# Optimization experiments

Measured on AMD Instinct MI355X. Metric: run time of the kernel, lower is better.

The kernel has to match this reference:

```python
import jax, jax.numpy as jnp
import numpy as np

N = 50000        # nodes
E = 800000       # edges
MUL = 32         # multiplicity per irrep (32x0e + 32x1o)
NSPEC = 4        # atom species (node_attrs one-hot width)
NBESSEL = 8      # edge_embedding basis size
HID = 8          # invariant_neurons
WNUM = 4 * MUL   # tp.weight_numel (4 'uvu' paths x 32)


def setup_inputs() -> dict:
    key = jax.random.key(0)
    ks = jax.random.split(key, 13)
    return {
        "edge_embedding": jax.random.normal(ks[0], (E, NBESSEL), jnp.float32),
        "node_attrs": jax.random.uniform(ks[1], (N, NSPEC), jnp.float32),
        "node_features": jax.random.normal(ks[2], (N, MUL * 4), jnp.float32),
        "edge_index": jax.random.randint(ks[3], (2, E), 0, N, jnp.int64),
        "edge_attrs": jax.random.normal(ks[4], (E, 4), jnp.float32),
        # linear_1 (per-irrep channel mixing)
        "W1_s": jax.random.normal(ks[5], (MUL, MUL), jnp.float32),
        "W1_v": jax.random.normal(ks[6], (MUL, MUL), jnp.float32),
        # fc: [8] -> [8] -> [128]
        "Wfc1": jax.random.normal(ks[7], (NBESSEL, HID), jnp.float32),
        "Wfc2": jax.random.normal(ks[8], (HID, WNUM), jnp.float32),
        # linear_2: 64x0e+64x1o -> 32x0e+32x1o
        "W2_s": jax.random.normal(ks[9], (2 * MUL, MUL), jnp.float32),
        "W2_v": jax.random.normal(ks[10], (2 * MUL, MUL), jnp.float32),
        # sc: FullyConnectedTensorProduct(32x0e+32x1o, 4x0e -> 32x0e+32x1o)
        "Wsc_s": jax.random.normal(ks[11], (MUL, NSPEC, MUL), jnp.float32),
        "Wsc_v": jax.random.normal(ks[12], (MUL, NSPEC, MUL), jnp.float32),
    }


def reference(edge_embedding, node_attrs, node_features, edge_index, edge_attrs,
              W1_s, W1_v, Wfc1, Wfc2, W2_s, W2_v, Wsc_s, Wsc_v):
    s = node_features[:, :MUL]                       # [N,32] 0e
    v = node_features[:, MUL:].reshape(N, MUL, 3)    # [N,32,3] 1o

    # self-connection: FullyConnectedTensorProduct(features, node_attrs)
    inv = 1.0 / np.sqrt(MUL * NSPEC).astype(np.float32)
    sc_s = jnp.einsum('nu,nz,uzv->nv', s, node_attrs, Wsc_s) * inv
    sc_v = jnp.einsum('nui,nz,uzv->nvi', v, node_attrs, Wsc_v) * inv

    # linear_1 (equivariant: mixes channels within each irrep)
    lin = np.float32(1.0 / np.sqrt(MUL))
    s1 = (s @ W1_s) * lin
    v1 = jnp.einsum('nui,uv->nvi', v, W1_v) * lin

    # fc MLP on edge_embedding -> per-edge TP weights [E,128]
    h = jax.nn.silu((edge_embedding @ Wfc1) * np.float32(1.0 / np.sqrt(NBESSEL)))
    w = (h @ Wfc2) * np.float32(1.0 / np.sqrt(HID))
    w0, w1, w2, w3 = w[:, :MUL], w[:, MUL:2*MUL], w[:, 2*MUL:3*MUL], w[:, 3*MUL:]

    ctr, nbr = edge_index[0], edge_index[1]
    xs = s1[nbr]            # [E,32] gathered scalars
    xv = v1[nbr]            # [E,32,3] gathered vectors
    es = edge_attrs[:, :1]  # [E,1]  edge 0e
    ev = edge_attrs[:, 1:4] # [E,3]  edge 1o

    # weighted CG tensor product ('uvu', per-edge weights)
    out_s0 = w0 * xs * es                                              # 0e x 0e -> 0e
    out_s3 = w3 * jnp.einsum('eui,ei->eu', xv, ev) * np.float32(1/np.sqrt(3))  # 1o x 1o -> 0e
    out_v1 = (w1 * xs)[:, :, None] * ev[:, None, :]                    # 0e x 1o -> 1o
    out_v2 = (w2 * es)[:, :, None] * xv                                # 1o x 0e -> 1o

    e_s = jnp.concatenate([out_s0, out_s3], axis=1)    # [E,64]
    e_v = jnp.concatenate([out_v1, out_v2], axis=1)    # [E,64,3]

    # scatter-sum back to center nodes
    n_s = jax.ops.segment_sum(e_s, ctr, num_segments=N)
    n_v = jax.ops.segment_sum(e_v.reshape(E, -1), ctr, num_segments=N).reshape(N, 2*MUL, 3)

    # linear_2 + residual self-connection
    lin2 = np.float32(1.0 / np.sqrt(2 * MUL))
    out_s = (n_s @ W2_s) * lin2 + sc_s
    out_v = jnp.einsum('nui,uv->nvi', n_v, W2_v) * lin2 + sc_v

    return jnp.concatenate([out_s, out_v.reshape(N, MUL * 3)], axis=1)
```

## Files before the change

### kernel.cpp

```cpp
#include <hip/hip_runtime.h>

#define N_NODES 50000
#define E_EDGES 800000
#define MUL 32
#define CAP 48

__device__ __forceinline__ unsigned bfpack2(float a, float b) {
    unsigned ua = __float_as_uint(a), ub = __float_as_uint(b);
    ua = (ua + 0x7FFFu + ((ua >> 16) & 1u)) >> 16;
    ub = (ub + 0x7FFFu + ((ub >> 16) & 1u)) >> 16;
    return ua | (ub << 16);
}
__device__ __forceinline__ float bflo(unsigned p) { return __uint_as_float(p << 16); }
__device__ __forceinline__ float bfhi(unsigned p) { return __uint_as_float(p & 0xFFFF0000u); }

__global__ __launch_bounds__(256) void edge_prep(
    const float* __restrict__ ee, const float* __restrict__ Wfc1,
    const int* __restrict__ ei, const float* __restrict__ ea,
    int* __restrict__ cnt, uint4* __restrict__ rec)
{
    __shared__ float sW[64];
    if (threadIdx.x < 64) sW[threadIdx.x] = Wfc1[threadIdx.x];
    __syncthreads();
    long long e = (long long)blockIdx.x * 256 + threadIdx.x;
    if (e >= E_EDGES) return;

    int c = ei[e];
    int nbr = ei[E_EDGES + e];
    int slot = atomicAdd(&cnt[c], 1);

    const float4* p = (const float4*)(ee + e * 8);
    float4 a = p[0], b = p[1];
    float emb[8] = {a.x, a.y, a.z, a.w, b.x, b.y, b.z, b.w};
    const float sfc = 0.35355339059327373f;
    float h[8];
#pragma unroll
    for (int k = 0; k < 8; ++k) {
        float acc = 0.f;
#pragma unroll
        for (int t = 0; t < 8; ++t) acc += emb[t] * sW[t * 8 + k];
        acc *= sfc;
        h[k] = acc / (1.f + __expf(-acc));
    }
    float4 av = ((const float4*)ea)[e];

    if (slot < CAP) {
        long long idx = (long long)(c * CAP + slot) * 2;
        uint4 A, B;
        A.x = (unsigned)nbr;
        A.y = bfpack2(h[0], h[1]); A.z = bfpack2(h[2], h[3]); A.w = bfpack2(h[4], h[5]);
        B.x = bfpack2(h[6], h[7]);
        B.y = bfpack2(av.x, av.y); B.z = bfpack2(av.z, av.w);
        B.w = 0u;
        rec[idx] = A;
        rec[idx + 1] = B;
    }
}

__global__ __launch_bounds__(512) void node_pre_sc(
    const float* __restrict__ nf, const float* __restrict__ attrs,
    const float* __restrict__ W1s, const float* __restrict__ W1v,
    const float* __restrict__ Wscs, const float* __restrict__ Wscv,
    uint2* __restrict__ xq, float* __restrict__ out)
{
    __shared__ float sW1s[1024];
    __shared__ float sW1v[1024];
    __shared__ float sWscs[4096];
    __shared__ float sWscv[4096];
    __shared__ float snf[16][128];
    __shared__ float sat[16][4];
    for (int i = threadIdx.x; i < 1024; i += 512) { sW1s[i] = W1s[i]; sW1v[i] = W1v[i]; }
    for (int i = threadIdx.x; i < 4096; i += 512) { sWscs[i] = Wscs[i]; sWscv[i] = Wscv[i]; }
    int g = threadIdx.x >> 5, v = threadIdx.x & 31;
    const float lin = 0.17677669529663687f;
    const float inv = 0.08838834764831845f;
    for (int node0 = blockIdx.x * 16; node0 < N_NODES; node0 += gridDim.x * 16) {
        __syncthreads();
        for (int i = threadIdx.x; i < 16 * 128; i += 512) {
            int nn = node0 + (i >> 7);
            snf[i >> 7][i & 127] = (nn < N_NODES) ? nf[(long long)nn * 128 + (i & 127)] : 0.f;
        }
        if (threadIdx.x < 64) {
            int nn = node0 + (threadIdx.x >> 2);
            sat[threadIdx.x >> 2][threadIdx.x & 3] = (nn < N_NODES) ? attrs[nn * 4 + (threadIdx.x & 3)] : 0.f;
        }
        __syncthreads();
        int n = node0 + g;
        if (n >= N_NODES) continue;
        float az0 = sat[g][0], az1 = sat[g][1], az2 = sat[g][2], az3 = sat[g][3];
        float acc_s = 0.f, a0 = 0.f, a1 = 0.f, a2 = 0.f;
        float scs = 0.f, scv0 = 0.f, scv1 = 0.f, scv2 = 0.f;
#pragma unroll
        for (int u = 0; u < 32; ++u) {
            float su = snf[g][u];
            float x0 = snf[g][32 + u * 3 + 0];
            float x1 = snf[g][32 + u * 3 + 1];
            float x2 = snf[g][32 + u * 3 + 2];
            acc_s += su * sW1s[u * 32 + v];
            float wv = sW1v[u * 32 + v];
            a0 += x0 * wv; a1 += x1 * wv; a2 += x2 * wv;
            int base = u * 128 + v;
            float cs = az0 * sWscs[base] + az1 * sWscs[base + 32] + az2 * sWscs[base + 64] + az3 * sWscs[base + 96];
            scs += su * cs;
            float cv = az0 * sWscv[base] + az1 * sWscv[base + 32] + az2 * sWscv[base + 64] + az3 * sWscv[base + 96];
            scv0 += x0 * cv; scv1 += x1 * cv; scv2 += x2 * cv;
        }
        uint2 q;
        q.x = bfpack2(acc_s * lin, a0 * lin);
        q.y = bfpack2(a1 * lin, a2 * lin);
        xq[n * 32 + v] = q;
        long long ob = (long long)n * 128;
        out[ob + v] = scs * inv;
        out[ob + 32 + v * 3 + 0] = scv0 * inv;
        out[ob + 32 + v * 3 + 1] = scv1 * inv;
        out[ob + 32 + v * 3 + 2] = scv2 * inv;
    }
}

__global__ __launch_bounds__(256, 6) void gather(
    const int* __restrict__ cnt, const uint4* __restrict__ rec,
    const uint2* __restrict__ xq, const float* __restrict__ Wfc2,
    float4* __restrict__ m4)
{
    int wid = threadIdx.x >> 6;
    int lane = threadIdx.x & 63;
    int u = lane & 31;
    int half = lane >> 5;
    const float sfc = 0.35355339059327373f;
    const float is3 = 0.5773502691896258f;
    float wf0[8], wf1[8], wf2[8], wf3[8];
#pragma unroll
    for (int t = 0; t < 8; ++t) {
        wf0[t] = Wfc2[t * 128 + u] * sfc;
        wf1[t] = Wfc2[t * 128 + 32 + u] * sfc;
        wf2[t] = Wfc2[t * 128 + 64 + u] * sfc;
        wf3[t] = Wfc2[t * 128 + 96 + u] * sfc;
    }
    for (int n = blockIdx.x * 4 + wid; n < N_NODES; n += gridDim.x * 4) {
        int deg = cnt[n];
        if (deg > CAP) deg = CAP;
        int T = (deg + 1) >> 1;
        long long base = (long long)n * CAP;
        int nbr_all = (lane < deg) ? (int)rec[(base + lane) * 2].x : 0;
        float as0 = 0.f, as3 = 0.f;
        float av10 = 0.f, av11 = 0.f, av12 = 0.f;
        float av20 = 0.f, av21 = 0.f, av22 = 0.f;
        uint4 A_c = {0, 0, 0, 0}, B_c = {0, 0, 0, 0};
        uint2 q_c = {0, 0};
        float m_c = 0.f;
        if (T > 0) {
            int j = half;
            m_c = (j < deg) ? 1.f : 0.f;
            int js = (j < deg) ? j : 0;
            int nbr = __shfl(nbr_all, js);
            A_c = rec[(base + js) * 2];
            B_c = rec[(base + js) * 2 + 1];
            q_c = xq[nbr * 32 + u];
        }
        for (int t = 0; t < T; ++t) {
            uint4 A_n = {0, 0, 0, 0}, B_n = {0, 0, 0, 0};
            uint2 q_n = {0, 0};
            float m_n = 0.f;
            if (t + 1 < T) {
                int j = 2 * (t + 1) + half;
                m_n = (j < deg) ? 1.f : 0.f;
                int js = (j < deg) ? j : 0;
                int nbr = __shfl(nbr_all, js);
                A_n = rec[(base + js) * 2];
                B_n = rec[(base + js) * 2 + 1];
                q_n = xq[nbr * 32 + u];
            }
            float hh[8] = {bflo(A_c.y), bfhi(A_c.y), bflo(A_c.z), bfhi(A_c.z),
                           bflo(A_c.w), bfhi(A_c.w), bflo(B_c.x), bfhi(B_c.x)};
            float w0 = 0.f, w1 = 0.f, w2 = 0.f, w3 = 0.f;
#pragma unroll
            for (int t8 = 0; t8 < 8; ++t8) {
                float ht = hh[t8];
                w0 += ht * wf0[t8];
                w1 += ht * wf1[t8];
                w2 += ht * wf2[t8];
                w3 += ht * wf3[t8];
            }
            w0 *= m_c; w1 *= m_c; w2 *= m_c; w3 *= m_c;
            float es  = bflo(B_c.y), ev0 = bfhi(B_c.y);
            float ev1 = bflo(B_c.z), ev2 = bfhi(B_c.z);
            float xs  = bflo(q_c.x), xv0 = bfhi(q_c.x);
            float xv1 = bflo(q_c.y), xv2 = bfhi(q_c.y);
            as0 += w0 * xs * es;
            as3 += w3 * (xv0 * ev0 + xv1 * ev1 + xv2 * ev2);
            float t1 = w1 * xs;
            float t2 = w2 * es;
            av10 += t1 * ev0; av11 += t1 * ev1; av12 += t1 * ev2;
            av20 += t2 * xv0; av21 += t2 * xv1; av22 += t2 * xv2;
            A_c = A_n; B_c = B_n; q_c = q_n; m_c = m_n;
        }
        as0  += __shfl_xor(as0, 32);
        as3  += __shfl_xor(as3, 32);
        av10 += __shfl_xor(av10, 32);
        av11 += __shfl_xor(av11, 32);
        av12 += __shfl_xor(av12, 32);
        av20 += __shfl_xor(av20, 32);
        av21 += __shfl_xor(av21, 32);
        av22 += __shfl_xor(av22, 32);
        if (half == 0) m4[(long long)n * 64 + u]      = make_float4(av10, av11, av12, as0);
        else           m4[(long long)n * 64 + 32 + u] = make_float4(av20, av21, av22, as3 * is3);
    }
}

__global__ __launch_bounds__(512) void node_post(
    const float4* __restrict__ m4,
    const float* __restrict__ W2s, const float* __restrict__ W2v,
    float* __restrict__ out)
{
    __shared__ float sW2s[2048];
    __shared__ float sW2v[2048];
    __shared__ float4 sm[16][64];
    for (int i = threadIdx.x; i < 2048; i += 512) { sW2s[i] = W2s[i]; sW2v[i] = W2v[i]; }
    int g = threadIdx.x >> 5, v = threadIdx.x & 31;
    const float lin2 = 0.125f;
    for (int node0 = blockIdx.x * 16; node0 < N_NODES; node0 += gridDim.x * 16) {
        __syncthreads();
        for (int i = threadIdx.x; i < 16 * 64; i += 512) {
            int nn = node0 + (i >> 6);
            sm[i >> 6][i & 63] = (nn < N_NODES) ? m4[(long long)nn * 64 + (i & 63)]
                                                : make_float4(0.f, 0.f, 0.f, 0.f);
        }
        __syncthreads();
        int n = node0 + g;
        if (n >= N_NODES) continue;
        float os = 0.f, ov0 = 0.f, ov1 = 0.f, ov2 = 0.f;
#pragma unroll 16
        for (int U = 0; U < 64; ++U) {
            float4 q = sm[g][U];
            os += q.w * sW2s[U * 32 + v];
            float wv = sW2v[U * 32 + v];
            ov0 += q.x * wv; ov1 += q.y * wv; ov2 += q.z * wv;
        }
        long long ob = (long long)n * 128;
        out[ob + v] += os * lin2;
        out[ob + 32 + v * 3 + 0] += ov0 * lin2;
        out[ob + 32 + v * 3 + 1] += ov1 * lin2;
        out[ob + 32 + v * 3 + 2] += ov2 * lin2;
    }
}

extern "C" void kernel_launch(void* const* d_in, const int* in_sizes, int n_in,
                              void* d_out, int out_size, void* d_ws, size_t ws_size,
                              hipStream_t stream) {
    const float* ee    = (const float*)d_in[0];
    const float* attrs = (const float*)d_in[1];
    const float* nf    = (const float*)d_in[2];
    const int*   ei    = (const int*)d_in[3];
    const float* ea    = (const float*)d_in[4];
    const float* W1s   = (const float*)d_in[5];
    const float* W1v   = (const float*)d_in[6];
    const float* Wfc1  = (const float*)d_in[7];
    const float* Wfc2  = (const float*)d_in[8];
    const float* W2s   = (const float*)d_in[9];
    const float* W2v   = (const float*)d_in[10];
    const float* Wscs  = (const float*)d_in[11];
    const float* Wscv  = (const float*)d_in[12];
    float* out = (float*)d_out;

    uint2*  xq  = (uint2*)d_ws;
    uint4*  rec = (uint4*)(xq + (size_t)N_NODES * 32);
    float4* m4  = (float4*)(rec + (size_t)N_NODES * CAP * 2);
    int*    cnt = (int*)(m4 + (size_t)N_NODES * 64);

    hipMemsetAsync(cnt, 0, (size_t)N_NODES * sizeof(int), stream);
    edge_prep<<<(E_EDGES + 255) / 256, 256, 0, stream>>>(ee, Wfc1, ei, ea, cnt, rec);
    node_pre_sc<<<768, 512, 0, stream>>>(nf, attrs, W1s, W1v, Wscs, Wscv, xq, out);
    gather<<<2048, 256, 0, stream>>>(cnt, rec, xq, Wfc2, m4);
    node_post<<<1024, 512, 0, stream>>>(m4, W2s, W2v, out);
}
```

Before: 416.4 us.

## Fold count reset into node kernel, deepen gather prefetch, transpose sc weights

```diff
diff --git a/kernel.cpp b/kernel.cpp
--- a/kernel.cpp
+++ b/kernel.cpp
@@ -13,6 +13,76 @@
 }
 __device__ __forceinline__ float bflo(unsigned p) { return __uint_as_float(p << 16); }
 __device__ __forceinline__ float bfhi(unsigned p) { return __uint_as_float(p & 0xFFFF0000u); }
+
+__global__ __launch_bounds__(512) void node_pre_sc(
+    const float* __restrict__ nf, const float* __restrict__ attrs,
+    const float* __restrict__ W1s, const float* __restrict__ W1v,
+    const float* __restrict__ Wscs, const float* __restrict__ Wscv,
+    uint2* __restrict__ xq, float* __restrict__ out, int* __restrict__ cnt)
+{
+    for (int i = blockIdx.x * 512 + threadIdx.x; i < N_NODES; i += gridDim.x * 512)
+        cnt[i] = 0;
+
+    __shared__ float sW1s[1024];
+    __shared__ float sW1v[1024];
+    __shared__ float sWscsT[4096];
+    __shared__ float sWscvT[4096];
+    __shared__ float snf[16][128];
+    __shared__ float sat[16][4];
+    for (int i = threadIdx.x; i < 1024; i += 512) { sW1s[i] = W1s[i]; sW1v[i] = W1v[i]; }
+    for (int i = threadIdx.x; i < 4096; i += 512) {
+        int u = i >> 7, rem = i & 127, z = rem >> 5, vv = rem & 31;
+        int t = ((u * 32 + vv) << 2) + z;
+        sWscsT[t] = Wscs[i];
+        sWscvT[t] = Wscv[i];
+    }
+    int g = threadIdx.x >> 5, v = threadIdx.x & 31;
+    const float lin = 0.17677669529663687f;
+    const float inv = 0.08838834764831845f;
+    for (int node0 = blockIdx.x * 16; node0 < N_NODES; node0 += gridDim.x * 16) {
+        __syncthreads();
+        for (int i = threadIdx.x; i < 16 * 128; i += 512) {
+            int nn = node0 + (i >> 7);
+            snf[i >> 7][i & 127] = (nn < N_NODES) ? nf[(long long)nn * 128 + (i & 127)] : 0.f;
+        }
+        if (threadIdx.x < 64) {
+            int nn = node0 + (threadIdx.x >> 2);
+            sat[threadIdx.x >> 2][threadIdx.x & 3] = (nn < N_NODES) ? attrs[nn * 4 + (threadIdx.x & 3)] : 0.f;
+        }
+        __syncthreads();
+        int n = node0 + g;
+        if (n >= N_NODES) continue;
+        float az0 = sat[g][0], az1 = sat[g][1], az2 = sat[g][2], az3 = sat[g][3];
+        float acc_s = 0.f, a0 = 0.f, a1 = 0.f, a2 = 0.f;
+        float scs = 0.f, scv0 = 0.f, scv1 = 0.f, scv2 = 0.f;
+#pragma unroll
+        for (int u = 0; u < 32; ++u) {
+            float su = snf[g][u];
+            float x0 = snf[g][32 + u * 3 + 0];
+            float x1 = snf[g][32 + u * 3 + 1];
+            float x2 = snf[g][32 + u * 3 + 2];
+            acc_s += su * sW1s[u * 32 + v];
+            float wv = sW1v[u * 32 + v];
+            a0 += x0 * wv; a1 += x1 * wv; a2 += x2 * wv;
+            int t = (u * 32 + v) << 2;
+            float4 cs4 = *(const float4*)&sWscsT[t];
+            float4 cv4 = *(const float4*)&sWscvT[t];
+            float cs = az0 * cs4.x + az1 * cs4.y + az2 * cs4.z + az3 * cs4.w;
+            scs += su * cs;
+            float cv = az0 * cv4.x + az1 * cv4.y + az2 * cv4.z + az3 * cv4.w;
+            scv0 += x0 * cv; scv1 += x1 * cv; scv2 += x2 * cv;
+        }
+        uint2 q;
+        q.x = bfpack2(acc_s * lin, a0 * lin);
+        q.y = bfpack2(a1 * lin, a2 * lin);
+        xq[n * 32 + v] = q;
+        long long ob = (long long)n * 128;
+        out[ob + v] = scs * inv;
+        out[ob + 32 + v * 3 + 0] = scv0 * inv;
+        out[ob + 32 + v * 3 + 1] = scv1 * inv;
+        out[ob + 32 + v * 3 + 2] = scv2 * inv;
+    }
+}
 
 __global__ __launch_bounds__(256) void edge_prep(
     const float* __restrict__ ee, const float* __restrict__ Wfc1,
@@ -57,66 +127,6 @@
     }
 }
 
-__global__ __launch_bounds__(512) void node_pre_sc(
-    const float* __restrict__ nf, const float* __restrict__ attrs,
-    const float* __restrict__ W1s, const float* __restrict__ W1v,
-    const float* __restrict__ Wscs, const float* __restrict__ Wscv,
-    uint2* __restrict__ xq, float* __restrict__ out)
-{
-    __shared__ float sW1s[1024];
-    __shared__ float sW1v[1024];
-    __shared__ float sWscs[4096];
-    __shared__ float sWscv[4096];
-    __shared__ float snf[16][128];
-    __shared__ float sat[16][4];
-    for (int i = threadIdx.x; i < 1024; i += 512) { sW1s[i] = W1s[i]; sW1v[i] = W1v[i]; }
-    for (int i = threadIdx.x; i < 4096; i += 512) { sWscs[i] = Wscs[i]; sWscv[i] = Wscv[i]; }
-    int g = threadIdx.x >> 5, v = threadIdx.x & 31;
-    const float lin = 0.17677669529663687f;
-    const float inv = 0.08838834764831845f;
-    for (int node0 = blockIdx.x * 16; node0 < N_NODES; node0 += gridDim.x * 16) {
-        __syncthreads();
-        for (int i = threadIdx.x; i < 16 * 128; i += 512) {
-            int nn = node0 + (i >> 7);
-            snf[i >> 7][i & 127] = (nn < N_NODES) ? nf[(long long)nn * 128 + (i & 127)] : 0.f;
-        }
-        if (threadIdx.x < 64) {
-            int nn = node0 + (threadIdx.x >> 2);
-            sat[threadIdx.x >> 2][threadIdx.x & 3] = (nn < N_NODES) ? attrs[nn * 4 + (threadIdx.x & 3)] : 0.f;
-        }
-        __syncthreads();
-        int n = node0 + g;
-        if (n >= N_NODES) continue;
-        float az0 = sat[g][0], az1 = sat[g][1], az2 = sat[g][2], az3 = sat[g][3];
-        float acc_s = 0.f, a0 = 0.f, a1 = 0.f, a2 = 0.f;
-        float scs = 0.f, scv0 = 0.f, scv1 = 0.f, scv2 = 0.f;
-#pragma unroll
-        for (int u = 0; u < 32; ++u) {
-            float su = snf[g][u];
-            float x0 = snf[g][32 + u * 3 + 0];
-            float x1 = snf[g][32 + u * 3 + 1];
-            float x2 = snf[g][32 + u * 3 + 2];
-            acc_s += su * sW1s[u * 32 + v];
-            float wv = sW1v[u * 32 + v];
-            a0 += x0 * wv; a1 += x1 * wv; a2 += x2 * wv;
-            int base = u * 128 + v;
-            float cs = az0 * sWscs[base] + az1 * sWscs[base + 32] + az2 * sWscs[base + 64] + az3 * sWscs[base + 96];
-            scs += su * cs;
-            float cv = az0 * sWscv[base] + az1 * sWscv[base + 32] + az2 * sWscv[base + 64] + az3 * sWscv[base + 96];
-            scv0 += x0 * cv; scv1 += x1 * cv; scv2 += x2 * cv;
-        }
-        uint2 q;
-        q.x = bfpack2(acc_s * lin, a0 * lin);
-        q.y = bfpack2(a1 * lin, a2 * lin);
-        xq[n * 32 + v] = q;
-        long long ob = (long long)n * 128;
-        out[ob + v] = scs * inv;
-        out[ob + 32 + v * 3 + 0] = scv0 * inv;
-        out[ob + 32 + v * 3 + 1] = scv1 * inv;
-        out[ob + 32 + v * 3 + 2] = scv2 * inv;
-    }
-}
-
 __global__ __launch_bounds__(256, 6) void gather(
     const int* __restrict__ cnt, const uint4* __restrict__ rec,
     const uint2* __restrict__ xq, const float* __restrict__ Wfc2,
@@ -134,44 +144,45 @@
         wf0[t] = Wfc2[t * 128 + u] * sfc;
         wf1[t] = Wfc2[t * 128 + 32 + u] * sfc;
         wf2[t] = Wfc2[t * 128 + 64 + u] * sfc;
-        wf3[t] = Wfc2[t * 128 + 96 + u] * sfc;
+        wf3[t] = Wfc2[t * 128 + 96 + u] * (sfc * is3);
     }
     for (int n = blockIdx.x * 4 + wid; n < N_NODES; n += gridDim.x * 4) {
         int deg = cnt[n];
         if (deg > CAP) deg = CAP;
         int T = (deg + 1) >> 1;
-        long long base = (long long)n * CAP;
-        int nbr_all = (lane < deg) ? (int)rec[(base + lane) * 2].x : 0;
+        long long base2 = (long long)n * CAP * 2;
         float as0 = 0.f, as3 = 0.f;
         float av10 = 0.f, av11 = 0.f, av12 = 0.f;
         float av20 = 0.f, av21 = 0.f, av22 = 0.f;
-        uint4 A_c = {0, 0, 0, 0}, B_c = {0, 0, 0, 0};
-        uint2 q_c = {0, 0};
-        float m_c = 0.f;
+        uint4 A0 = {0,0,0,0}, B0 = {0,0,0,0}, A1 = {0,0,0,0}, B1 = {0,0,0,0};
+        uint2 q0 = {0, 0};
+        float m0 = 0.f, m1 = 0.f;
         if (T > 0) {
             int j = half;
-            m_c = (j < deg) ? 1.f : 0.f;
-            int js = (j < deg) ? j : 0;
-            int nbr = __shfl(nbr_all, js);
-            A_c = rec[(base + js) * 2];
-            B_c = rec[(base + js) * 2 + 1];
-            q_c = xq[nbr * 32 + u];
-        }
+            m0 = (j < deg) ? 1.f : 0.f;
+            long long r = base2 + ((j < deg) ? j : 0) * 2;
+            A0 = rec[r]; B0 = rec[r + 1];
+        }
+        if (T > 1) {
+            int j = 2 + half;
+            m1 = (j < deg) ? 1.f : 0.f;
+            long long r = base2 + ((j < deg) ? j : 0) * 2;
+            A1 = rec[r]; B1 = rec[r + 1];
+        }
+        if (T > 0) q0 = xq[(int)A0.x * 32 + u];
         for (int t = 0; t < T; ++t) {
-            uint4 A_n = {0, 0, 0, 0}, B_n = {0, 0, 0, 0};
-            uint2 q_n = {0, 0};
-            float m_n = 0.f;
-            if (t + 1 < T) {
-                int j = 2 * (t + 1) + half;
-                m_n = (j < deg) ? 1.f : 0.f;
-                int js = (j < deg) ? j : 0;
-                int nbr = __shfl(nbr_all, js);
-                A_n = rec[(base + js) * 2];
-                B_n = rec[(base + js) * 2 + 1];
-                q_n = xq[nbr * 32 + u];
+            uint4 A2 = {0,0,0,0}, B2 = {0,0,0,0};
+            uint2 q1 = {0, 0};
+            float m2 = 0.f;
+            if (t + 2 < T) {
+                int j = 2 * (t + 2) + half;
+                m2 = (j < deg) ? 1.f : 0.f;
+                long long r = base2 + ((j < deg) ? j : 0) * 2;
+                A2 = rec[r]; B2 = rec[r + 1];
             }
-            float hh[8] = {bflo(A_c.y), bfhi(A_c.y), bflo(A_c.z), bfhi(A_c.z),
-                           bflo(A_c.w), bfhi(A_c.w), bflo(B_c.x), bfhi(B_c.x)};
+            if (t + 1 < T) q1 = xq[(int)A1.x * 32 + u];
+            float hh[8] = {bflo(A0.y), bfhi(A0.y), bflo(A0.z), bfhi(A0.z),
+                           bflo(A0.w), bfhi(A0.w), bflo(B0.x), bfhi(B0.x)};
             float w0 = 0.f, w1 = 0.f, w2 = 0.f, w3 = 0.f;
 #pragma unroll
             for (int t8 = 0; t8 < 8; ++t8) {
@@ -181,18 +192,19 @@
                 w2 += ht * wf2[t8];
                 w3 += ht * wf3[t8];
             }
-            w0 *= m_c; w1 *= m_c; w2 *= m_c; w3 *= m_c;
-            float es  = bflo(B_c.y), ev0 = bfhi(B_c.y);
-            float ev1 = bflo(B_c.z), ev2 = bfhi(B_c.z);
-            float xs  = bflo(q_c.x), xv0 = bfhi(q_c.x);
-            float xv1 = bflo(q_c.y), xv2 = bfhi(q_c.y);
+            w0 *= m0; w1 *= m0; w2 *= m0; w3 *= m0;
+            float es  = bflo(B0.y), ev0 = bfhi(B0.y);
+            float ev1 = bflo(B0.z), ev2 = bfhi(B0.z);
+            float xs  = bflo(q0.x), xv0 = bfhi(q0.x);
+            float xv1 = bflo(q0.y), xv2 = bfhi(q0.y);
             as0 += w0 * xs * es;
             as3 += w3 * (xv0 * ev0 + xv1 * ev1 + xv2 * ev2);
             float t1 = w1 * xs;
             float t2 = w2 * es;
             av10 += t1 * ev0; av11 += t1 * ev1; av12 += t1 * ev2;
             av20 += t2 * xv0; av21 += t2 * xv1; av22 += t2 * xv2;
-            A_c = A_n; B_c = B_n; q_c = q_n; m_c = m_n;
+            A0 = A1; B0 = B1; q0 = q1; m0 = m1;
+            A1 = A2; B1 = B2; m1 = m2;
         }
         as0  += __shfl_xor(as0, 32);
         as3  += __shfl_xor(as3, 32);
@@ -203,7 +215,7 @@
         av21 += __shfl_xor(av21, 32);
         av22 += __shfl_xor(av22, 32);
         if (half == 0) m4[(long long)n * 64 + u]      = make_float4(av10, av11, av12, as0);
-        else           m4[(long long)n * 64 + 32 + u] = make_float4(av20, av21, av22, as3 * is3);
+        else           m4[(long long)n * 64 + 32 + u] = make_float4(av20, av21, av22, as3);
     }
 }
 
@@ -267,9 +279,8 @@
     float4* m4  = (float4*)(rec + (size_t)N_NODES * CAP * 2);
     int*    cnt = (int*)(m4 + (size_t)N_NODES * 64);
 
-    hipMemsetAsync(cnt, 0, (size_t)N_NODES * sizeof(int), stream);
+    node_pre_sc<<<768, 512, 0, stream>>>(nf, attrs, W1s, W1v, Wscs, Wscv, xq, out, cnt);
     edge_prep<<<(E_EDGES + 255) / 256, 256, 0, stream>>>(ee, Wfc1, ei, ea, cnt, rec);
-    node_pre_sc<<<768, 512, 0, stream>>>(nf, attrs, W1s, W1v, Wscs, Wscv, xq, out);
     gather<<<2048, 256, 0, stream>>>(cnt, rec, xq, Wfc2, m4);
     node_post<<<1024, 512, 0, stream>>>(m4, W2s, W2v, out);
 }
```

Result: slower. 510.4 us (+22.6%).
